# Kernel optimization log

Measured on AMD Instinct MI355X. Metric: run time of the kernel, lower is better.

Reference implementation:

```python
import jax, jax.numpy as jnp
import numpy as np
from jax import lax

BETA = 0.9
THRESHOLD = 1.0
NUM_STEPS = 32
SLOPE = 25.0  # snntorch surrogate.fast_sigmoid default slope


def heaviside(x):
    return (x > 0).astype(x.dtype)


def setup_inputs() -> dict:
    key = jax.random.key(0)
    k1, k2, k3, k4 = jax.random.split(key, 4)
    B, D = 2048, 1024
    latent = jax.random.normal(k1, (B, D), dtype=jnp.float32)
    W = jax.random.normal(k2, (D, D), dtype=jnp.float32) * (1.0 / np.sqrt(D))
    b = jax.random.normal(k3, (D,), dtype=jnp.float32) * 0.01
    gain = jnp.asarray(-0.9, dtype=jnp.float32)
    return {"latent": latent, "W": W, "b": b, "gain": gain}


def reference(latent, W, b, gain):
    # projection: current = latent @ W.T + b (nn.Linear semantics)
    current = jnp.einsum("bd,ed->be", latent, W) + b

    def step(mem, _):
        # snntorch Leaky, reset_mechanism='subtract':
        #   reset based on previous membrane (detached)
        reset = lax.stop_gradient(heaviside(mem - THRESHOLD))
        mem = BETA * mem + current - reset * THRESHOLD
        spk = heaviside(mem - THRESHOLD)
        return mem, spk

    mem0 = jnp.zeros_like(current)
    _, spikes = lax.scan(step, mem0, None, length=NUM_STEPS)  # [T, B, D]
    spike_tensor = jnp.transpose(spikes, (1, 0, 2))  # [B, T, D]

    scale = 0.4 * jax.nn.sigmoid(gain)
    updated = jax.nn.relu(latent + scale * spike_tensor.mean(axis=1))
    return (updated, spike_tensor, lax.stop_gradient(scale))
```

## Files before the change

### kernel.cpp

```cpp
#include <hip/hip_runtime.h>
#include <math.h>

#define FMUL(a,b) __fmul_rn((a),(b))
#define FADD(a,b) __fadd_rn((a),(b))
#define FSUB(a,b) __fsub_rn((a),(b))

#define BB 2048
#define DD 1024
#define TT 32
#define TS 64
#define KB 32
#define NSLAB (DD / KB)
#define HALF  (NSLAB / 2)

__global__ __launch_bounds__(256) void lif_fused_kernel(
    const float* __restrict__ latent,
    const float* __restrict__ W,
    const float* __restrict__ bias,
    const float* __restrict__ gainp,
    float* __restrict__ out)
{
    __shared__ float4 As4[2][KB / 4][TS];
    __shared__ float4 Ws4[2][KB / 4][TS];

    const int tid = threadIdx.x;
    const int tx = tid & 15;
    const int ty = tid >> 4;
    const int e0 = blockIdx.x * TS;
    const int b0 = blockIdx.y * TS;

    const int lrow = tid >> 2;
    const int lf4  = tid & 3;

    const float* aptr = latent + (size_t)(b0 + lrow) * DD + lf4 * 4;
    const float* wptr = W      + (size_t)(e0 + lrow) * DD + lf4 * 4;

    float tot[4][4];
    float acc[4][4];
#pragma unroll
    for (int i = 0; i < 4; ++i)
#pragma unroll
        for (int j = 0; j < 4; ++j) acc[i][j] = 0.0f;

    float4 a0 = *(const float4*)(aptr +  0);
    float4 a1 = *(const float4*)(aptr + 16);
    float4 w0 = *(const float4*)(wptr +  0);
    float4 w1 = *(const float4*)(wptr + 16);

    int p = 0;
    for (int s = 0; s < NSLAB; ++s) {
        As4[p][lf4    ][lrow] = a0;
        As4[p][lf4 + 4][lrow] = a1;
        Ws4[p][lf4    ][lrow] = w0;
        Ws4[p][lf4 + 4][lrow] = w1;
        __syncthreads();

        if (s + 1 < NSLAB) {
            const int k0 = (s + 1) * KB;
            a0 = *(const float4*)(aptr + k0);
            a1 = *(const float4*)(aptr + k0 + 16);
            w0 = *(const float4*)(wptr + k0);
            w1 = *(const float4*)(wptr + k0 + 16);
        }

        if (s == HALF) {
#pragma unroll
            for (int i = 0; i < 4; ++i)
#pragma unroll
                for (int j = 0; j < 4; ++j) { tot[i][j] = acc[i][j]; acc[i][j] = 0.0f; }
        }

#pragma unroll
        for (int sub = 0; sub < KB / 4; ++sub) {
            float4 a4[4], w4[4];
#pragma unroll
            for (int i = 0; i < 4; ++i) a4[i] = As4[p][sub][ty * 4 + i];
#pragma unroll
            for (int j = 0; j < 4; ++j) w4[j] = Ws4[p][sub][tx * 4 + j];
#pragma unroll
            for (int j = 0; j < 4; ++j)
#pragma unroll
                for (int i = 0; i < 4; ++i) {
                    float a = acc[i][j];
                    a = fmaf(a4[i].x, w4[j].x, a);
                    a = fmaf(a4[i].y, w4[j].y, a);
                    a = fmaf(a4[i].z, w4[j].z, a);
                    a = fmaf(a4[i].w, w4[j].w, a);
                    acc[i][j] = a;
                }
        }
        p ^= 1;
    }

    float4 bv = *(const float4*)&bias[e0 + tx * 4];
    float cur[4][4];
#pragma unroll
    for (int i = 0; i < 4; ++i) {
        cur[i][0] = FADD(FADD(tot[i][0], acc[i][0]), bv.x);
        cur[i][1] = FADD(FADD(tot[i][1], acc[i][1]), bv.y);
        cur[i][2] = FADD(FADD(tot[i][2], acc[i][2]), bv.z);
        cur[i][3] = FADD(FADD(tot[i][3], acc[i][3]), bv.w);
    }

    float mem[4][4];
    int cnt[4][4];
#pragma unroll
    for (int i = 0; i < 4; ++i)
#pragma unroll
        for (int j = 0; j < 4; ++j) { mem[i][j] = 0.0f; cnt[i][j] = 0; }

    float* spk_base = out + (size_t)BB * DD;
    const int colf = e0 + tx * 4;

    for (int t = 0; t < TT; ++t) {
#pragma unroll
        for (int i = 0; i < 4; ++i) {
            const int row = b0 + ty * 4 + i;
            float4 s;
#pragma unroll
            for (int j = 0; j < 4; ++j) {
                float m = mem[i][j];
                float r = (m > 1.0f) ? 1.0f : 0.0f;
                m = FSUB(FADD(FMUL(0.9f, m), cur[i][j]), r);
                mem[i][j] = m;
                int fired = (m > 1.0f) ? 1 : 0;
                cnt[i][j] += fired;
                ((float*)&s)[j] = (float)fired;
            }
            *(float4*)&spk_base[(size_t)row * TT * DD + (size_t)t * DD + colf] = s;
        }
    }

    const float g = gainp[0];
    const float scale = 0.4f * (1.0f / (1.0f + expf(-g)));

#pragma unroll
    for (int i = 0; i < 4; ++i) {
        const int row = b0 + ty * 4 + i;
        float4 lv = *(const float4*)&latent[(size_t)row * DD + colf];
        float4 u;
#pragma unroll
        for (int j = 0; j < 4; ++j) {
            float mean = (float)cnt[i][j] * 0.03125f;
            float tterm = FMUL(scale, mean);
            float v = FADD(((const float*)&lv)[j], tterm);
            ((float*)&u)[j] = v > 0.0f ? v : 0.0f;
        }
        *(float4*)&out[(size_t)row * DD + colf] = u;
    }

    if (blockIdx.x == 0 && blockIdx.y == 0 && tid == 0) {
        out[(size_t)BB * DD + (size_t)BB * TT * DD] = scale;
    }
}

extern "C" void kernel_launch(void* const* d_in, const int* in_sizes, int n_in,
                              void* d_out, int out_size, void* d_ws, size_t ws_size,
                              hipStream_t stream) {
    (void)in_sizes; (void)n_in; (void)d_ws; (void)ws_size; (void)out_size;
    const float* latent = (const float*)d_in[0];
    const float* W      = (const float*)d_in[1];
    const float* bias   = (const float*)d_in[2];
    const float* gain   = (const float*)d_in[3];
    float* out = (float*)d_out;

    dim3 grid(DD / TS, BB / TS);
    dim3 block(256);
    lif_fused_kernel<<<grid, block, 0, stream>>>(latent, W, bias, gain, out);
}
```

Baseline: 125.0 us.

## Restructure GEMM tile to wave-per-row-group with scalar latent loads

Changes the block tile from 64x64 to 32 rows by 64 columns, with each wavefront owning 8 batch rows and each lane one output column. The latent operand is no longer staged in shared memory. Since the row index is wave-uniform via readfirstlane, latent values can be fetched through scalar loads, and only W is staged in LDS. Spike stores become per-lane scalar writes that stay coalesced across each wave. The point is to cut LDS traffic and raise block count, at the cost of less register-level reuse per thread (8 outputs instead of 16) and reliance on scalar-cache bandwidth for the A operand.

```diff
diff --git a/kernel.cpp b/kernel.cpp
--- a/kernel.cpp
+++ b/kernel.cpp
@@ -8,10 +8,11 @@
 #define BB 2048
 #define DD 1024
 #define TT 32
-#define TS 64
+#define BM 32
+#define BN 64
 #define KB 32
 #define NSLAB (DD / KB)
-#define HALF  (NSLAB / 2)
+#define HALFS (NSLAB / 2)
 
 __global__ __launch_bounds__(256) void lif_fused_kernel(
     const float* __restrict__ latent,
@@ -20,138 +21,101 @@
     const float* __restrict__ gainp,
     float* __restrict__ out)
 {
-    __shared__ float4 As4[2][KB / 4][TS];
-    __shared__ float4 Ws4[2][KB / 4][TS];
+    __shared__ float4 Ws4[2][KB / 4][BN];
 
-    const int tid = threadIdx.x;
-    const int tx = tid & 15;
-    const int ty = tid >> 4;
-    const int e0 = blockIdx.x * TS;
-    const int b0 = blockIdx.y * TS;
+    const int tid  = threadIdx.x;
+    const int lane = tid & 63;
+    const int wid  = __builtin_amdgcn_readfirstlane(tid >> 6);
 
-    const int lrow = tid >> 2;
-    const int lf4  = tid & 3;
+    const int e0 = blockIdx.x * BN;
+    const int b0 = blockIdx.y * BM;
+    const int e  = e0 + lane;
+    const int r0 = b0 + wid * 8;
 
-    const float* aptr = latent + (size_t)(b0 + lrow) * DD + lf4 * 4;
-    const float* wptr = W      + (size_t)(e0 + lrow) * DD + lf4 * 4;
+    const int srow = tid >> 2;
+    const int sf   = tid & 3;
+    const float* wptr = W + (size_t)(e0 + srow) * DD + sf * 4;
 
-    float tot[4][4];
-    float acc[4][4];
+    const float* __restrict__ abase = latent + (size_t)r0 * DD;
+
+    float acc[8], tot[8];
 #pragma unroll
-    for (int i = 0; i < 4; ++i)
-#pragma unroll
-        for (int j = 0; j < 4; ++j) acc[i][j] = 0.0f;
+    for (int i = 0; i < 8; ++i) { acc[i] = 0.0f; tot[i] = 0.0f; }
 
-    float4 a0 = *(const float4*)(aptr +  0);
-    float4 a1 = *(const float4*)(aptr + 16);
-    float4 w0 = *(const float4*)(wptr +  0);
+    float4 w0 = *(const float4*)(wptr);
     float4 w1 = *(const float4*)(wptr + 16);
 
     int p = 0;
     for (int s = 0; s < NSLAB; ++s) {
-        As4[p][lf4    ][lrow] = a0;
-        As4[p][lf4 + 4][lrow] = a1;
-        Ws4[p][lf4    ][lrow] = w0;
-        Ws4[p][lf4 + 4][lrow] = w1;
+        Ws4[p][sf    ][srow] = w0;
+        Ws4[p][sf + 4][srow] = w1;
         __syncthreads();
 
         if (s + 1 < NSLAB) {
             const int k0 = (s + 1) * KB;
-            a0 = *(const float4*)(aptr + k0);
-            a1 = *(const float4*)(aptr + k0 + 16);
             w0 = *(const float4*)(wptr + k0);
             w1 = *(const float4*)(wptr + k0 + 16);
         }
 
-        if (s == HALF) {
+        if (s == HALFS) {
 #pragma unroll
-            for (int i = 0; i < 4; ++i)
-#pragma unroll
-                for (int j = 0; j < 4; ++j) { tot[i][j] = acc[i][j]; acc[i][j] = 0.0f; }
+            for (int i = 0; i < 8; ++i) { tot[i] = acc[i]; acc[i] = 0.0f; }
         }
 
+        const float* __restrict__ aS = abase + s * KB;
 #pragma unroll
-        for (int sub = 0; sub < KB / 4; ++sub) {
-            float4 a4[4], w4[4];
+        for (int kg = 0; kg < KB / 4; ++kg) {
+            float4 w4 = Ws4[p][kg][lane];
 #pragma unroll
-            for (int i = 0; i < 4; ++i) a4[i] = As4[p][sub][ty * 4 + i];
-#pragma unroll
-            for (int j = 0; j < 4; ++j) w4[j] = Ws4[p][sub][tx * 4 + j];
-#pragma unroll
-            for (int j = 0; j < 4; ++j)
-#pragma unroll
-                for (int i = 0; i < 4; ++i) {
-                    float a = acc[i][j];
-                    a = fmaf(a4[i].x, w4[j].x, a);
-                    a = fmaf(a4[i].y, w4[j].y, a);
-                    a = fmaf(a4[i].z, w4[j].z, a);
-                    a = fmaf(a4[i].w, w4[j].w, a);
-                    acc[i][j] = a;
-                }
+            for (int i = 0; i < 8; ++i) {
+                const float* ai = aS + i * DD + kg * 4;
+                float a = acc[i];
+                a = fmaf(ai[0], w4.x, a);
+                a = fmaf(ai[1], w4.y, a);
+                a = fmaf(ai[2], w4.z, a);
+                a = fmaf(ai[3], w4.w, a);
+                acc[i] = a;
+            }
         }
         p ^= 1;
     }
 
-    float4 bv = *(const float4*)&bias[e0 + tx * 4];
-    float cur[4][4];
+    const float bv = bias[e];
+    float cur[8], mem[8];
+    int cnt[8];
 #pragma unroll
-    for (int i = 0; i < 4; ++i) {
-        cur[i][0] = FADD(FADD(tot[i][0], acc[i][0]), bv.x);
-        cur[i][1] = FADD(FADD(tot[i][1], acc[i][1]), bv.y);
-        cur[i][2] = FADD(FADD(tot[i][2], acc[i][2]), bv.z);
-        cur[i][3] = FADD(FADD(tot[i][3], acc[i][3]), bv.w);
+    for (int i = 0; i < 8; ++i) {
+        cur[i] = FADD(FADD(tot[i], acc[i]), bv);
+        mem[i] = 0.0f;
+        cnt[i] = 0;
     }
 
-    float mem[4][4];
-    int cnt[4][4];
-#pragma unroll
-    for (int i = 0; i < 4; ++i)
-#pragma unroll
-        for (int j = 0; j < 4; ++j) { mem[i][j] = 0.0f; cnt[i][j] = 0; }
-
-    float* spk_base = out + (size_t)BB * DD;
-    const int colf = e0 + tx * 4;
-
+    float* spk = out + (size_t)BB * DD;
     for (int t = 0; t < TT; ++t) {
 #pragma unroll
-        for (int i = 0; i < 4; ++i) {
-            const int row = b0 + ty * 4 + i;
-            float4 s;
-#pragma unroll
-            for (int j = 0; j < 4; ++j) {
-                float m = mem[i][j];
-                float r = (m > 1.0f) ? 1.0f : 0.0f;
-                m = FSUB(FADD(FMUL(0.9f, m), cur[i][j]), r);
-                mem[i][j] = m;
-                int fired = (m > 1.0f) ? 1 : 0;
-                cnt[i][j] += fired;
-                ((float*)&s)[j] = (float)fired;
-            }
-            *(float4*)&spk_base[(size_t)row * TT * DD + (size_t)t * DD + colf] = s;
+        for (int i = 0; i < 8; ++i) {
+            float m = mem[i];
+            float r = (m > 1.0f) ? 1.0f : 0.0f;
+            m = FSUB(FADD(FMUL(0.9f, m), cur[i]), r);
+            mem[i] = m;
+            int f = (m > 1.0f) ? 1 : 0;
+            cnt[i] += f;
+            spk[((size_t)(r0 + i) * TT + t) * DD + e] = (float)f;
         }
     }
 
     const float g = gainp[0];
     const float scale = 0.4f * (1.0f / (1.0f + expf(-g)));
-
 #pragma unroll
-    for (int i = 0; i < 4; ++i) {
-        const int row = b0 + ty * 4 + i;
-        float4 lv = *(const float4*)&latent[(size_t)row * DD + colf];
-        float4 u;
-#pragma unroll
-        for (int j = 0; j < 4; ++j) {
-            float mean = (float)cnt[i][j] * 0.03125f;
-            float tterm = FMUL(scale, mean);
-            float v = FADD(((const float*)&lv)[j], tterm);
-            ((float*)&u)[j] = v > 0.0f ? v : 0.0f;
-        }
-        *(float4*)&out[(size_t)row * DD + colf] = u;
+    for (int i = 0; i < 8; ++i) {
+        float lv = latent[(size_t)(r0 + i) * DD + e];
+        float mean = (float)cnt[i] * 0.03125f;
+        float v = FADD(lv, FMUL(scale, mean));
+        out[(size_t)(r0 + i) * DD + e] = v > 0.0f ? v : 0.0f;
     }
 
-    if (blockIdx.x == 0 && blockIdx.y == 0 && tid == 0) {
+    if (blockIdx.x == 0 && blockIdx.y == 0 && tid == 0)
         out[(size_t)BB * DD + (size_t)BB * TT * DD] = scale;
-    }
 }
 
 extern "C" void kernel_launch(void* const* d_in, const int* in_sizes, int n_in,
@@ -164,7 +128,7 @@
     const float* gain   = (const float*)d_in[3];
     float* out = (float*)d_out;
 
-    dim3 grid(DD / TS, BB / TS);
+    dim3 grid(DD / BN, BB / BM);
     dim3 block(256);
     lif_fused_kernel<<<grid, block, 0, stream>>>(latent, W, bias, gain, out);
 }
```

After: 191.8 us. +53.4%, slower.
